# Performance work log

Hardware: AMD Instinct MI355X
Metric: run time of the kernel (lower is better)

The kernel has to match this reference:

```python
import jax, jax.numpy as jnp
import numpy as np

H, W = 32, 56
CK, CV = 64, 512
N = 16 * H * W  # long + work memory fully populated: 16 frames of H*W entries
TOP_K = 30


def setup_inputs() -> dict:
    key = jax.random.key(0)
    k1, k2, k3, k4, k5 = jax.random.split(key, 5)
    return {
        "q_key": jax.random.normal(k1, (1, CK, H, W), dtype=jnp.float32),
        "q_selection": jax.random.uniform(k2, (1, CK, H, W), dtype=jnp.float32),
        "mem_key": jax.random.normal(k3, (1, CK, N), dtype=jnp.float32),
        "mem_shrinkage": jax.random.uniform(k4, (1, N, 1), dtype=jnp.float32),
        "mem_value": jax.random.normal(k5, (2, CV, N), dtype=jnp.float32),
    }


def reference(q_key, q_selection, mem_key, mem_shrinkage, mem_value):
    b, ck, h, w = q_key.shape
    hw = h * w
    qk = q_key.reshape(1, ck, hw)          # [1, CK, HW]
    qs = q_selection.reshape(1, ck, hw)    # [1, CK, HW]

    mk = jnp.swapaxes(mem_key, 1, 2)       # [1, N, CK]
    # negative weighted squared L2 distance via matmul algebra
    a_sq = jnp.matmul(mk * mk, qs)                    # [1, N, HW]
    two_ab = 2.0 * jnp.matmul(mk, qk * qs)            # [1, N, HW]
    b_sq = jnp.sum(qs * qk * qk, axis=1, keepdims=True)  # [1, 1, HW]
    sim = (-a_sq + two_ab - b_sq) * mem_shrinkage / jnp.sqrt(jnp.float32(ck))  # [1, N, HW]

    # topk over the memory axis (dim=1), softmax over selected entries, scatter back
    simT = jnp.swapaxes(sim, 1, 2)                    # [1, HW, N]
    vals, idx = jax.lax.top_k(simT, TOP_K)            # [1, HW, K]
    x_exp = jnp.exp(vals)
    x_exp = x_exp / jnp.sum(x_exp, axis=-1, keepdims=True)
    i0 = jnp.arange(1)[:, None, None]
    i1 = jnp.arange(hw)[None, :, None]
    affT = jnp.zeros_like(simT).at[i0, i1, idx].set(x_exp)  # [1, HW, N]
    affinity = jnp.swapaxes(affT, 1, 2)               # [1, N, HW]

    out = jnp.matmul(mem_value, affinity)             # [2, CV, HW] (batch-broadcast)
    return out.reshape(2, CV, h, w)
```

## Files before the change

kernel.cpp:

```cpp
#include <hip/hip_runtime.h>
#include <math.h>

#define HW      1792
#define NMEM    28672
#define NCHUNK  3584
#define TOPK    30
#define CTARGET 64
#define BINS    2048
#define BSHIFT  20
#define VCACHE  2048
#define BCAP    768
#define SIMB    448
#define WPS     7

typedef __attribute__((ext_vector_type(8))) short bf16x8;
typedef __attribute__((ext_vector_type(8))) unsigned short u16x8;
typedef __attribute__((ext_vector_type(4))) float f32x4;
typedef __attribute__((ext_vector_type(4))) _Float16 h4;

static __device__ __forceinline__ unsigned short f2bf(float v) {
  unsigned b = __float_as_uint(v);
  return (unsigned short)((b + 0x7FFFu + ((b >> 16) & 1u)) >> 16);
}
static __device__ __forceinline__ float bf2f(unsigned short h) {
  return __uint_as_float(((unsigned)h) << 16);
}
static __device__ __forceinline__ unsigned fkey(float v) {
  return __float_as_uint(-v) & 0x7FFFFFFFu;
}
static __device__ __forceinline__ void gl_lds16(const void* g, void* l) {
  __builtin_amdgcn_global_load_lds(
      (const __attribute__((address_space(1))) unsigned*)g,
      (__attribute__((address_space(3))) unsigned*)l, 16, 0, 0);
}

__global__ __launch_bounds__(256)
void k_prep_b(const float* __restrict__ mk, const float* __restrict__ shr_in,
              unsigned short* __restrict__ Bh,
              float* __restrict__ mkT, float* __restrict__ shr_s)
{
  const int n = blockIdx.x * 256 + threadIdx.x;
  shr_s[n] = shr_in[n] * 0.125f;
  for (int cb = 0; cb < 64; cb += 8) {
    u16x8 h1, h2;
    float vv[8];
    #pragma unroll
    for (int j = 0; j < 8; ++j) {
      float v = mk[(size_t)(cb + j) * NMEM + n];
      vv[j] = v;
      h1[j] = f2bf(v);
      h2[j] = f2bf(v * v);
    }
    const int s = cb >> 3;
    *reinterpret_cast<u16x8*>(&Bh[((size_t)s * NMEM + n) * 8])       = h1;
    *reinterpret_cast<u16x8*>(&Bh[((size_t)(s + 8) * NMEM + n) * 8]) = h2;
    *reinterpret_cast<float4*>(&mkT[(size_t)n * 64 + cb])     = make_float4(vv[0], vv[1], vv[2], vv[3]);
    *reinterpret_cast<float4*>(&mkT[(size_t)n * 64 + cb + 4]) = make_float4(vv[4], vv[5], vv[6], vv[7]);
  }
}

__global__ __launch_bounds__(256)
void k_prep_u(const float* __restrict__ q_key, const float* __restrict__ q_sel,
              unsigned short* __restrict__ Uh, unsigned short* __restrict__ Ul,
              float* __restrict__ bsq)
{
  const int p = blockIdx.x * 256 + threadIdx.x;
  float bs = 0.f;
  for (int cb = 0; cb < 64; cb += 8) {
    u16x8 h1, l1, h2, l2;
    #pragma unroll
    for (int j = 0; j < 8; ++j) {
      int c = cb + j;
      float k = q_key[(size_t)c * HW + p];
      float s = q_sel[(size_t)c * HW + p];
      float u = 2.f * k * s;
      float w = -s;
      bs = fmaf(s * k, k, bs);
      unsigned short h = f2bf(u); h1[j] = h; l1[j] = f2bf(u - bf2f(h));
      unsigned short g = f2bf(w); h2[j] = g; l2[j] = f2bf(w - bf2f(g));
    }
    const int s = cb >> 3;
    *reinterpret_cast<u16x8*>(&Uh[((size_t)s * HW + p) * 8])       = h1;
    *reinterpret_cast<u16x8*>(&Ul[((size_t)s * HW + p) * 8])       = l1;
    *reinterpret_cast<u16x8*>(&Uh[((size_t)(s + 8) * HW + p) * 8]) = h2;
    *reinterpret_cast<u16x8*>(&Ul[((size_t)(s + 8) * HW + p) * 8]) = l2;
  }
  bsq[p] = bs;
}

__global__ __launch_bounds__(256, 2)
void k_sim(const unsigned short* __restrict__ Uh, const unsigned short* __restrict__ Ul,
           const unsigned short* __restrict__ Bh,
           const float* __restrict__ bsq, const float* __restrict__ shr_s,
           float* __restrict__ pmax)
{
  __shared__ char smem[65536] __attribute__((aligned(16)));
  const int tid = threadIdx.x;
  const int wid = tid >> 6, lane = tid & 63;
  const int lr = lane & 15, lg = lane >> 4;
  const int pb = blockIdx.x % 14, st = blockIdx.x / 14;
  const int pw = pb * 128 + wid * 32;
  const int w0 = st * WPS;

  bf16x8 a0h[4], a0l[4], a1h[4], a1l[4];
  #pragma unroll
  for (int t = 0; t < 4; ++t) {
    const size_t e0 = ((size_t)(t * 4 + lg) * HW + pw + lr) * 8;
    const size_t e1 = e0 + 16 * 8;
    a0h[t] = *reinterpret_cast<const bf16x8*>(&Uh[e0]);
    a0l[t] = *reinterpret_cast<const bf16x8*>(&Ul[e0]);
    a1h[t] = *reinterpret_cast<const bf16x8*>(&Uh[e1]);
    a1l[t] = *reinterpret_cast<const bf16x8*>(&Ul[e1]);
  }
  float bq[2][4];
  #pragma unroll
  for (int pt = 0; pt < 2; ++pt)
    #pragma unroll
    for (int r = 0; r < 4; ++r) bq[pt][r] = bsq[pw + pt * 16 + 4 * lg + r];

  auto stage = [&](int buf, int i) {
    const int n0 = (w0 + i) * 128;
    #pragma unroll
    for (int j = 0; j < 8; ++j) {
      const int idx = j * 256 + tid;
      const int s = idx >> 7, rr = idx & 127;
      gl_lds16((const char*)Bh + ((size_t)s * NMEM + n0 + rr) * 16,
               smem + buf * 32768 + idx * 16);
    }
  };

  stage(0, 0);
  int buf = 0;
  for (int i = 0; i < WPS; ++i) {
    __syncthreads();
    if (i + 1 < WPS) stage(buf ^ 1, i + 1);

    f32x4 acc[2][8];
    #pragma unroll
    for (int a = 0; a < 2; ++a)
      #pragma unroll
      for (int b = 0; b < 8; ++b) acc[a][b] = (f32x4){0.f, 0.f, 0.f, 0.f};

    const short* lb = (const short*)(smem + buf * 32768);
    #pragma unroll
    for (int t = 0; t < 4; ++t) {
      #pragma unroll
      for (int nt = 0; nt < 8; ++nt) {
        bf16x8 bh = *reinterpret_cast<const bf16x8*>(
            &lb[((t * 4 + lg) * 128 + nt * 16 + lr) * 8]);
        acc[0][nt] = __builtin_amdgcn_mfma_f32_16x16x32_bf16(a0h[t], bh, acc[0][nt], 0, 0, 0);
        acc[0][nt] = __builtin_amdgcn_mfma_f32_16x16x32_bf16(a0l[t], bh, acc[0][nt], 0, 0, 0);
        acc[1][nt] = __builtin_amdgcn_mfma_f32_16x16x32_bf16(a1h[t], bh, acc[1][nt], 0, 0, 0);
        acc[1][nt] = __builtin_amdgcn_mfma_f32_16x16x32_bf16(a1l[t], bh, acc[1][nt], 0, 0, 0);
      }
    }

    const int wgl = w0 + i;
    const int n0 = wgl * 128;
    float shv[8];
    #pragma unroll
    for (int nt = 0; nt < 8; ++nt) shv[nt] = shr_s[n0 + nt * 16 + lr];
    #pragma unroll
    for (int pt = 0; pt < 2; ++pt) {
      #pragma unroll
      for (int r = 0; r < 4; ++r) {
        float mx = -INFINITY;
        #pragma unroll
        for (int nt = 0; nt < 8; ++nt)
          mx = fmaxf(mx, (acc[pt][nt][r] - bq[pt][r]) * shv[nt]);
        pmax[(size_t)(pw + pt * 16 + 4 * lg + r) * NCHUNK + wgl * 16 + lr] = mx;
      }
    }
    buf ^= 1;
  }
}

struct SelS {
  int            hist[BINS];
  unsigned short chl[NCHUNK];
  float          vcache[VCACHE];
  float          sqk[64], sqs[64];
  unsigned       au[64];
  int            ai[64];
  unsigned       bu[BCAP];
  int            bi[BCAP];
  float          fv[32];
  int            fi[32];
  float          ew[32];
  int            lsum[256];
  int            wsum[4];
  int            sB, sNA, cA, cB, sSC;
  float          sSum;
};
union SMemU {
  SelS  sel;
  float tt[64][65];
};

__device__ __forceinline__ void find_cross(SelS& s, int tid, int target)
{
  const int base = tid * (BINS / 256);
  int ls = 0;
  #pragma unroll
  for (int k = 0; k < BINS / 256; ++k) ls += s.hist[base + k];
  s.lsum[tid] = ls;
  __syncthreads();
  int lane = tid & 63, wv = tid >> 6;
  int v = ls;
  #pragma unroll
  for (int off = 1; off < 64; off <<= 1) {
    int t = __shfl_up(v, off);
    if (lane >= off) v += t;
  }
  if (lane == 63) s.wsum[wv] = v;
  __syncthreads();
  int wo = 0;
  for (int k = 0; k < wv; ++k) wo += s.wsum[k];
  int run = wo + v - ls;
  #pragma unroll 1
  for (int k = 0; k < BINS / 256; ++k) {
    int h = s.hist[base + k];
    if (run < target && run + h >= target) { s.sB = base + k; s.sNA = run; }
    run += h;
  }
  __syncthreads();
}

__global__ __launch_bounds__(256, 4)
void k_selT(const float* __restrict__ pmax, const float* __restrict__ mkT,
            const float* __restrict__ q_key, const float* __restrict__ q_sel,
            const float* __restrict__ shr_s,
            float* __restrict__ wgt, int* __restrict__ widx,
            const float* __restrict__ mv, _Float16* __restrict__ mvT)
{
  __shared__ SMemU sm;
  const int tid = threadIdx.x;

  int pix = -1, tb = -1;
  if (gridDim.x > HW) {
    const int g = blockIdx.x / 5, r = blockIdx.x % 5;
    if (r == 0) pix = g; else tb = g * 4 + (r - 1);
  } else {
    pix = blockIdx.x;
  }

  if (tb >= 0) {
    const int n0 = (tb % 448) * 64, ch0 = (tb / 448) * 64;
    for (int i = tid; i < 64 * 16; i += 256) {
      int r = i >> 4, c4 = (i & 15) << 2;
      float4 v = *reinterpret_cast<const float4*>(&mv[(size_t)(ch0 + r) * NMEM + n0 + c4]);
      sm.tt[r][c4] = v.x; sm.tt[r][c4 + 1] = v.y;
      sm.tt[r][c4 + 2] = v.z; sm.tt[r][c4 + 3] = v.w;
    }
    __syncthreads();
    for (int i = tid; i < 64 * 16; i += 256) {
      int r = i >> 4, c4 = (i & 15) << 2;
      h4 hv = {(_Float16)sm.tt[c4][r], (_Float16)sm.tt[c4 + 1][r],
               (_Float16)sm.tt[c4 + 2][r], (_Float16)sm.tt[c4 + 3][r]};
      *reinterpret_cast<h4*>(&mvT[(size_t)(n0 + r) * 1024 + ch0 + c4]) = hv;
    }
    return;
  }

  SelS& s = sm.sel;
  if (tid < 64) {
    s.sqk[tid] = q_key[(size_t)tid * HW + pix];
    s.sqs[tid] = q_sel[(size_t)tid * HW + pix];
  }
  for (int i = tid; i < BINS; i += 256) s.hist[i] = 0;
  if (tid == 0) { s.sSC = 0; s.cA = 0; s.cB = 0; }
  __syncthreads();

  float m[NCHUNK / 256];
  const float* pm = pmax + (size_t)pix * NCHUNK;
  #pragma unroll
  for (int j = 0; j < NCHUNK / 256; ++j) m[j] = pm[tid + 256 * j];
  #pragma unroll
  for (int j = 0; j < NCHUNK / 256; ++j) atomicAdd(&s.hist[fkey(m[j]) >> BSHIFT], 1);
  __syncthreads();
  find_cross(s, tid, CTARGET);
  {
    const int B = s.sB;
    #pragma unroll
    for (int j = 0; j < NCHUNK / 256; ++j)
      if ((int)(fkey(m[j]) >> BSHIFT) <= B) {
        int k = atomicAdd(&s.sSC, 1);
        s.chl[k] = (unsigned short)(tid + 256 * j);
      }
  }
  __syncthreads();
  const int NC = s.sSC * 8;
  for (int i = tid; i < BINS; i += 256) s.hist[i] = 0;
  __syncthreads();

  const float4* sqk4 = reinterpret_cast<const float4*>(s.sqk);
  const float4* sqs4 = reinterpret_cast<const float4*>(s.sqs);

  for (int c = tid; c < NC; c += 256) {
    const int cc = s.chl[c >> 3];
    const int n = ((cc >> 4) << 7) + (cc & 15) + ((c & 7) << 4);
    const float4* mr = reinterpret_cast<const float4*>(mkT + (size_t)n * 64);
    float sv = 0.f;
    #pragma unroll
    for (int j = 0; j < 16; ++j) {
      float4 q = mr[j], k4 = sqk4[j], s4 = sqs4[j];
      float d0 = q.x - k4.x, d1 = q.y - k4.y, d2 = q.z - k4.z, d3 = q.w - k4.w;
      sv = fmaf(s4.x * d0, d0, sv); sv = fmaf(s4.y * d1, d1, sv);
      sv = fmaf(s4.z * d2, d2, sv); sv = fmaf(s4.w * d3, d3, sv);
    }
    float v = -sv * shr_s[n];
    if (c < VCACHE) s.vcache[c] = v;
    atomicAdd(&s.hist[fkey(v) >> BSHIFT], 1);
  }
  __syncthreads();
  find_cross(s, tid, TOPK);

  {
    const int B2 = s.sB;
    for (int c = tid; c < NC; c += 256) {
      const int cc = s.chl[c >> 3];
      const int n = ((cc >> 4) << 7) + (cc & 15) + ((c & 7) << 4);
      float v;
      if (c < VCACHE) v = s.vcache[c];
      else {
        const float4* mr = reinterpret_cast<const float4*>(mkT + (size_t)n * 64);
        float sv = 0.f;
        #pragma unroll
        for (int j = 0; j < 16; ++j) {
          float4 q = mr[j], k4 = sqk4[j], s4 = sqs4[j];
          float d0 = q.x - k4.x, d1 = q.y - k4.y, d2 = q.z - k4.z, d3 = q.w - k4.w;
          sv = fmaf(s4.x * d0, d0, sv); sv = fmaf(s4.y * d1, d1, sv);
          sv = fmaf(s4.z * d2, d2, sv); sv = fmaf(s4.w * d3, d3, sv);
        }
        v = -sv * shr_s[n];
      }
      unsigned u = fkey(v);
      int bin = (int)(u >> BSHIFT);
      if (bin < B2)       { int k = atomicAdd(&s.cA, 1); s.au[k] = u; s.ai[k] = n; }
      else if (bin == B2) { int k = atomicAdd(&s.cB, 1); if (k < BCAP) { s.bu[k] = u; s.bi[k] = n; } }
    }
  }
  __syncthreads();
  {
    const int nAv = s.cA, mm = (s.cB < BCAP ? s.cB : BCAP), need = TOPK - nAv;
    for (int t = tid; t < mm; t += 256) {
      unsigned u = s.bu[t]; int id = s.bi[t];
      int r = 0;
      for (int k2 = 0; k2 < mm; ++k2) {
        unsigned uk = s.bu[k2];
        r += (uk < u) || (uk == u && s.bi[k2] < id);
      }
      if (r < need) { s.au[nAv + r] = u; s.ai[nAv + r] = id; }
    }
  }
  __syncthreads();

  if (tid < TOPK) {
    unsigned u = s.au[tid]; int id = s.ai[tid];
    int r = 0;
    for (int k2 = 0; k2 < TOPK; ++k2) {
      unsigned uk = s.au[k2];
      r += (uk < u) || (uk == u && s.ai[k2] < id);
    }
    s.fv[r] = -__uint_as_float(u); s.fi[r] = id;
  }
  __syncthreads();
  if (tid < 32) {
    float e = (tid < TOPK) ? expf(s.fv[tid]) : 0.f;
    if (tid < TOPK) s.ew[tid] = e;
    float ss = e;
    #pragma unroll
    for (int off = 16; off > 0; off >>= 1) ss += __shfl_down(ss, off);
    if (tid == 0) s.sSum = ss;
  }
  __syncthreads();
  if (tid < TOPK) {
    wgt [(size_t)pix * 32 + tid] = s.ew[tid] / s.sSum;
    widx[(size_t)pix * 32 + tid] = s.fi[tid];
  }
}

__global__ __launch_bounds__(256)
void k_transpose_h(const float* __restrict__ mv, _Float16* __restrict__ mvT)
{
  __shared__ float t[64][65];
  const int n0 = blockIdx.x * 64, ch0 = blockIdx.y * 64;
  const int tid = threadIdx.x;
  for (int i = tid; i < 64 * 16; i += 256) {
    int r = i >> 4, c4 = (i & 15) << 2;
    float4 v = *reinterpret_cast<const float4*>(&mv[(size_t)(ch0 + r) * NMEM + n0 + c4]);
    t[r][c4] = v.x; t[r][c4 + 1] = v.y; t[r][c4 + 2] = v.z; t[r][c4 + 3] = v.w;
  }
  __syncthreads();
  for (int i = tid; i < 64 * 16; i += 256) {
    int r = i >> 4, c4 = (i & 15) << 2;
    h4 hv = {(_Float16)t[c4][r], (_Float16)t[c4 + 1][r],
             (_Float16)t[c4 + 2][r], (_Float16)t[c4 + 3][r]};
    *reinterpret_cast<h4*>(&mvT[(size_t)(n0 + r) * 1024 + ch0 + c4]) = hv;
  }
}

__global__ __launch_bounds__(256)
void k_gather_h(const _Float16* __restrict__ mvT, const float* __restrict__ wgt,
                const int* __restrict__ widx, float* __restrict__ out)
{
  __shared__ float sw[8][TOPK];
  __shared__ int   si[8][TOPK];
  __shared__ float sbuf[256][9];
  const int p0 = blockIdx.x * 8, chg = blockIdx.y * 256;
  const int tid = threadIdx.x;

  for (int i = tid; i < 8 * TOPK; i += 256) {
    int q = i / TOPK, k = i - q * TOPK;
    sw[q][k] = wgt [(size_t)(p0 + q) * 32 + k];
    si[q][k] = widx[(size_t)(p0 + q) * 32 + k];
  }
  __syncthreads();

  const int ch = chg + tid;
  #pragma unroll 2
  for (int q = 0; q < 8; ++q) {
    float a = 0.f;
    #pragma unroll
    for (int k = 0; k < TOPK; ++k)
      a = fmaf(sw[q][k], (float)mvT[(size_t)si[q][k] * 1024 + ch], a);
    sbuf[tid][q] = a;
  }
  __syncthreads();

  for (int i = tid; i < 256 * 8; i += 256) {
    int cl = i >> 3, q = i & 7;
    out[(size_t)(chg + cl) * HW + p0 + q] = sbuf[cl][q];
  }
}

__global__ __launch_bounds__(256)
void k_gather_f(const float* __restrict__ src, const float* __restrict__ wgt,
                const int* __restrict__ widx, float* __restrict__ out,
                long n_stride, long ch_stride)
{
  __shared__ float sw[8][TOPK];
  __shared__ int   si[8][TOPK];
  __shared__ float sbuf[256][9];
  const int p0 = blockIdx.x * 8, chg = blockIdx.y * 256;
  const int tid = threadIdx.x;

  for (int i = tid; i < 8 * TOPK; i += 256) {
    int q = i / TOPK, k = i - q * TOPK;
    sw[q][k] = wgt [(size_t)(p0 + q) * 32 + k];
    si[q][k] = widx[(size_t)(p0 + q) * 32 + k];
  }
  __syncthreads();

  const int ch = chg + tid;
  #pragma unroll 2
  for (int q = 0; q < 8; ++q) {
    float a = 0.f;
    #pragma unroll
    for (int k = 0; k < TOPK; ++k)
      a = fmaf(sw[q][k], src[(size_t)si[q][k] * n_stride + (size_t)ch * ch_stride], a);
    sbuf[tid][q] = a;
  }
  __syncthreads();

  for (int i = tid; i < 256 * 8; i += 256) {
    int cl = i >> 3, q = i & 7;
    out[(size_t)(chg + cl) * HW + p0 + q] = sbuf[cl][q];
  }
}

extern "C" void kernel_launch(void* const* d_in, const int* in_sizes, int n_in,
                              void* d_out, int out_size, void* d_ws, size_t ws_size,
                              hipStream_t stream)
{
  (void)in_sizes; (void)n_in; (void)out_size;
  const float* q_key     = (const float*)d_in[0];
  const float* q_sel     = (const float*)d_in[1];
  const float* mem_key   = (const float*)d_in[2];
  const float* mem_shr   = (const float*)d_in[3];
  const float* mem_value = (const float*)d_in[4];
  float* out = (float*)d_out;

  char* ws = (char*)d_ws;
  size_t off = 0;
  auto alloc = [&](size_t b) { size_t c = off; off = (off + b + 255) & ~(size_t)255; return c; };
  size_t o_w   = alloc((size_t)HW * 32 * 4);
  size_t o_wi  = alloc((size_t)HW * 32 * 4);
  size_t o_pr  = off;
  size_t o_bh  = alloc((size_t)NMEM * 128 * 2);
  size_t o_uh  = alloc((size_t)HW * 128 * 2);
  size_t o_ul  = alloc((size_t)HW * 128 * 2);
  size_t o_bsq = alloc((size_t)HW * 4);
  size_t o_shr = alloc((size_t)NMEM * 4);
  size_t o_mkT = alloc((size_t)NMEM * 64 * 4);
  size_t o_pm  = alloc((size_t)HW * NCHUNK * 4);
  size_t o_end = off;

  float*          wg   = (float*)(ws + o_w);
  int*            wi   = (int*)  (ws + o_wi);
  unsigned short* Bh   = (unsigned short*)(ws + o_bh);
  unsigned short* Uh   = (unsigned short*)(ws + o_uh);
  unsigned short* Ul   = (unsigned short*)(ws + o_ul);
  float*          bsq  = (float*)(ws + o_bsq);
  float*          shr  = (float*)(ws + o_shr);
  float*          mkT  = (float*)(ws + o_mkT);
  float*          pmx  = (float*)(ws + o_pm);

  const size_t mvh_sz = (size_t)NMEM * 1024 * 2;

  k_prep_b<<<NMEM / 256, 256, 0, stream>>>(mem_key, mem_shr, Bh, mkT, shr);
  k_prep_u<<<HW / 256, 256, 0, stream>>>(q_key, q_sel, Uh, Ul, bsq);
  k_sim<<<SIMB, 256, 0, stream>>>(Uh, Ul, Bh, bsq, shr, pmx);

  if (ws_size >= o_end + mvh_sz) {
    _Float16* mvT = (_Float16*)(ws + o_end);
    k_selT<<<HW * 5, 256, 0, stream>>>(pmx, mkT, q_key, q_sel, shr,
                                       wg, wi, mem_value, mvT);
    k_gather_h<<<dim3(HW / 8, 4), 256, 0, stream>>>(mvT, wg, wi, out);
  } else {
    k_selT<<<HW, 256, 0, stream>>>(pmx, mkT, q_key, q_sel, shr,
                                   wg, wi, mem_value, nullptr);
    if (ws_size >= o_pr + mvh_sz) {
      _Float16* mvT = (_Float16*)(ws + o_pr);
      k_transpose_h<<<dim3(NMEM / 64, 16), 256, 0, stream>>>(mem_value, mvT);
      k_gather_h<<<dim3(HW / 8, 4), 256, 0, stream>>>(mvT, wg, wi, out);
    } else {
      k_gather_f<<<dim3(HW / 8, 4), 256, 0, stream>>>(
          mem_value, wg, wi, out, 1, NMEM);
    }
  }
}
```

Before: 143.5 us.

## Add second-level radix histogram pass to top-k selection and split histograms by wave

Refines both candidate-chunk selection and final top-k threshold with a second 11-bit radix histogram over the boundary bin. This shrinks the candidate set (fewer chunks rescored) and the tie bucket sorted by the quadratic rank loop. Histograms are duplicated per wave pair to reduce atomic contention, and find_cross keeps bins in registers. It adds extra passes, barriers and histogram clears, and shrinks the value cache, which may force more recomputation of distances from global memory.

```diff
diff --git a/kernel.cpp b/kernel.cpp
--- a/kernel.cpp
+++ b/kernel.cpp
@@ -7,9 +7,10 @@
 #define TOPK    30
 #define CTARGET 64
 #define BINS    2048
-#define BSHIFT  20
-#define VCACHE  2048
-#define BCAP    768
+#define L1SHIFT 20
+#define L2SHIFT 9
+#define VCACHE  1024
+#define BCAP    512
 #define SIMB    448
 #define WPS     7
 
@@ -176,7 +177,7 @@
 }
 
 struct SelS {
-  int            hist[BINS];
+  int            hist[2][BINS];
   unsigned short chl[NCHUNK];
   float          vcache[VCACHE];
   float          sqk[64], sqs[64];
@@ -200,9 +201,13 @@
 __device__ __forceinline__ void find_cross(SelS& s, int tid, int target)
 {
   const int base = tid * (BINS / 256);
+  int hv[8];
   int ls = 0;
   #pragma unroll
-  for (int k = 0; k < BINS / 256; ++k) ls += s.hist[base + k];
+  for (int k = 0; k < 8; ++k) {
+    hv[k] = s.hist[0][base + k] + s.hist[1][base + k];
+    ls += hv[k];
+  }
   s.lsum[tid] = ls;
   __syncthreads();
   int lane = tid & 63, wv = tid >> 6;
@@ -217,13 +222,18 @@
   int wo = 0;
   for (int k = 0; k < wv; ++k) wo += s.wsum[k];
   int run = wo + v - ls;
-  #pragma unroll 1
-  for (int k = 0; k < BINS / 256; ++k) {
-    int h = s.hist[base + k];
-    if (run < target && run + h >= target) { s.sB = base + k; s.sNA = run; }
-    run += h;
-  }
-  __syncthreads();
+  #pragma unroll
+  for (int k = 0; k < 8; ++k) {
+    if (run < target && run + hv[k] >= target) { s.sB = base + k; s.sNA = run; }
+    run += hv[k];
+  }
+  __syncthreads();
+}
+
+__device__ __forceinline__ void clear_hist(SelS& s, int tid)
+{
+  #pragma unroll
+  for (int k = 0; k < 2 * BINS / 256; ++k) (&s.hist[0][0])[tid + 256 * k] = 0;
 }
 
 __global__ __launch_bounds__(256, 4)
@@ -263,11 +273,13 @@
   }
 
   SelS& s = sm.sel;
+  const int hc = (tid >> 6) & 1;
+
   if (tid < 64) {
     s.sqk[tid] = q_key[(size_t)tid * HW + pix];
     s.sqs[tid] = q_sel[(size_t)tid * HW + pix];
   }
-  for (int i = tid; i < BINS; i += 256) s.hist[i] = 0;
+  clear_hist(s, tid);
   if (tid == 0) { s.sSC = 0; s.cA = 0; s.cB = 0; }
   __syncthreads();
 
@@ -276,21 +288,38 @@
   #pragma unroll
   for (int j = 0; j < NCHUNK / 256; ++j) m[j] = pm[tid + 256 * j];
   #pragma unroll
-  for (int j = 0; j < NCHUNK / 256; ++j) atomicAdd(&s.hist[fkey(m[j]) >> BSHIFT], 1);
+  for (int j = 0; j < NCHUNK / 256; ++j)
+    atomicAdd(&s.hist[hc][fkey(m[j]) >> L1SHIFT], 1);
   __syncthreads();
   find_cross(s, tid, CTARGET);
-  {
-    const int B = s.sB;
-    #pragma unroll
-    for (int j = 0; j < NCHUNK / 256; ++j)
-      if ((int)(fkey(m[j]) >> BSHIFT) <= B) {
-        int k = atomicAdd(&s.sSC, 1);
-        s.chl[k] = (unsigned short)(tid + 256 * j);
-      }
+  const int B1 = s.sB, nA1 = s.sNA;
+  clear_hist(s, tid);
+  __syncthreads();
+
+  #pragma unroll
+  for (int j = 0; j < NCHUNK / 256; ++j) {
+    unsigned u = fkey(m[j]);
+    if ((int)(u >> L1SHIFT) == B1)
+      atomicAdd(&s.hist[hc][(u >> L2SHIFT) & (BINS - 1)], 1);
+  }
+  __syncthreads();
+  find_cross(s, tid, CTARGET - nA1);
+  const int Bs1 = s.sB;
+
+  #pragma unroll
+  for (int j = 0; j < NCHUNK / 256; ++j) {
+    unsigned u = fkey(m[j]);
+    int bin = (int)(u >> L1SHIFT);
+    bool keep = (bin < B1) ||
+                (bin == B1 && (int)((u >> L2SHIFT) & (BINS - 1)) <= Bs1);
+    if (keep) {
+      int k = atomicAdd(&s.sSC, 1);
+      s.chl[k] = (unsigned short)(tid + 256 * j);
+    }
   }
   __syncthreads();
   const int NC = s.sSC * 8;
-  for (int i = tid; i < BINS; i += 256) s.hist[i] = 0;
+  clear_hist(s, tid);
   __syncthreads();
 
   const float4* sqk4 = reinterpret_cast<const float4*>(s.sqk);
@@ -310,34 +339,66 @@
     }
     float v = -sv * shr_s[n];
     if (c < VCACHE) s.vcache[c] = v;
-    atomicAdd(&s.hist[fkey(v) >> BSHIFT], 1);
+    atomicAdd(&s.hist[hc][fkey(v) >> L1SHIFT], 1);
   }
   __syncthreads();
   find_cross(s, tid, TOPK);
-
-  {
-    const int B2 = s.sB;
-    for (int c = tid; c < NC; c += 256) {
+  const int B2 = s.sB, nA2 = s.sNA;
+  clear_hist(s, tid);
+  __syncthreads();
+
+  for (int c = tid; c < NC; c += 256) {
+    float v;
+    if (c < VCACHE) v = s.vcache[c];
+    else {
       const int cc = s.chl[c >> 3];
       const int n = ((cc >> 4) << 7) + (cc & 15) + ((c & 7) << 4);
-      float v;
-      if (c < VCACHE) v = s.vcache[c];
-      else {
-        const float4* mr = reinterpret_cast<const float4*>(mkT + (size_t)n * 64);
-        float sv = 0.f;
-        #pragma unroll
-        for (int j = 0; j < 16; ++j) {
-          float4 q = mr[j], k4 = sqk4[j], s4 = sqs4[j];
-          float d0 = q.x - k4.x, d1 = q.y - k4.y, d2 = q.z - k4.z, d3 = q.w - k4.w;
-          sv = fmaf(s4.x * d0, d0, sv); sv = fmaf(s4.y * d1, d1, sv);
-          sv = fmaf(s4.z * d2, d2, sv); sv = fmaf(s4.w * d3, d3, sv);
-        }
-        v = -sv * shr_s[n];
+      const float4* mr = reinterpret_cast<const float4*>(mkT + (size_t)n * 64);
+      float sv = 0.f;
+      #pragma unroll
+      for (int j = 0; j < 16; ++j) {
+        float4 q = mr[j], k4 = sqk4[j], s4 = sqs4[j];
+        float d0 = q.x - k4.x, d1 = q.y - k4.y, d2 = q.z - k4.z, d3 = q.w - k4.w;
+        sv = fmaf(s4.x * d0, d0, sv); sv = fmaf(s4.y * d1, d1, sv);
+        sv = fmaf(s4.z * d2, d2, sv); sv = fmaf(s4.w * d3, d3, sv);
       }
-      unsigned u = fkey(v);
-      int bin = (int)(u >> BSHIFT);
-      if (bin < B2)       { int k = atomicAdd(&s.cA, 1); s.au[k] = u; s.ai[k] = n; }
-      else if (bin == B2) { int k = atomicAdd(&s.cB, 1); if (k < BCAP) { s.bu[k] = u; s.bi[k] = n; } }
+      v = -sv * shr_s[n];
+    }
+    unsigned u = fkey(v);
+    if ((int)(u >> L1SHIFT) == B2)
+      atomicAdd(&s.hist[hc][(u >> L2SHIFT) & (BINS - 1)], 1);
+  }
+  __syncthreads();
+  find_cross(s, tid, TOPK - nA2);
+  const int Bs2 = s.sB;
+
+  for (int c = tid; c < NC; c += 256) {
+    float v;
+    if (c < VCACHE) v = s.vcache[c];
+    else {
+      const int cc = s.chl[c >> 3];
+      const int n = ((cc >> 4) << 7) + (cc & 15) + ((c & 7) << 4);
+      const float4* mr = reinterpret_cast<const float4*>(mkT + (size_t)n * 64);
+      float sv = 0.f;
+      #pragma unroll
+      for (int j = 0; j < 16; ++j) {
+        float4 q = mr[j], k4 = sqk4[j], s4 = sqs4[j];
+        float d0 = q.x - k4.x, d1 = q.y - k4.y, d2 = q.z - k4.z, d3 = q.w - k4.w;
+        sv = fmaf(s4.x * d0, d0, sv); sv = fmaf(s4.y * d1, d1, sv);
+        sv = fmaf(s4.z * d2, d2, sv); sv = fmaf(s4.w * d3, d3, sv);
+      }
+      v = -sv * shr_s[n];
+    }
+    const int cc = s.chl[c >> 3];
+    const int n = ((cc >> 4) << 7) + (cc & 15) + ((c & 7) << 4);
+    unsigned u = fkey(v);
+    int bin = (int)(u >> L1SHIFT);
+    if (bin < B2) {
+      int k = atomicAdd(&s.cA, 1); s.au[k] = u; s.ai[k] = n;
+    } else if (bin == B2) {
+      int sub = (int)((u >> L2SHIFT) & (BINS - 1));
+      if (sub < Bs2)       { int k = atomicAdd(&s.cA, 1); s.au[k] = u; s.ai[k] = n; }
+      else if (sub == Bs2) { int k = atomicAdd(&s.cB, 1); if (k < BCAP) { s.bu[k] = u; s.bi[k] = n; } }
     }
   }
   __syncthreads();
```

Measured after the change: 199.6 us. 39.1% more time.
